# Kernel optimization log

Hardware: AMD Instinct MI355X
Metric: run time of the kernel (lower is better)

The kernel has to match this reference:

```python
import jax, jax.numpy as jnp
import numpy as np

N_NODES = 50000
N_EDGES = 800000
NFEAT, NHID, NCLASS = 256, 64, 2


def _deg_norm(idx, n_nodes, dtype):
    deg = jax.ops.segment_sum(jnp.ones(idx.shape[0], dtype=dtype), idx, num_segments=n_nodes)
    return jax.lax.rsqrt(jnp.maximum(deg, 1.0))


def gcn_layer(x, W, b, src, dst, n_nodes):
    # DGL GraphConv, norm='both': h = D_in^{-1/2} * Agg( D_out^{-1/2} * x ) W + b
    # weight applied before aggregation (in_feats >= out_feats path); math-equivalent.
    norm_src = _deg_norm(src, n_nodes, x.dtype)  # out-degree norm of source nodes
    norm_dst = _deg_norm(dst, n_nodes, x.dtype)  # in-degree norm of dest nodes
    h = (x * norm_src[:, None]) @ W              # [N, out]
    agg = jax.ops.segment_sum(h[src], dst, num_segments=n_nodes)  # gather + scatter-add
    return agg * norm_dst[:, None] + b


def setup_inputs() -> dict:
    key = jax.random.key(0)
    k1, k2, k3, k4, k5, k6, k7 = jax.random.split(key, 7)
    x = jax.random.normal(k1, (N_NODES, NFEAT), dtype=jnp.float32)
    src = jax.random.randint(k2, (N_EDGES,), 0, N_NODES, dtype=jnp.int64)
    dst = jax.random.randint(k3, (N_EDGES,), 0, N_NODES, dtype=jnp.int64)
    # Glorot-style init like DGL GraphConv
    W1 = jax.random.normal(k4, (NFEAT, NHID), dtype=jnp.float32) * (2.0 / (NFEAT + NHID)) ** 0.5
    b1 = jnp.zeros((NHID,), dtype=jnp.float32)
    W2 = jax.random.normal(k5, (NHID, NCLASS), dtype=jnp.float32) * (2.0 / (NHID + NCLASS)) ** 0.5
    b2 = jnp.zeros((NCLASS,), dtype=jnp.float32)
    return {"x": x, "src": src, "dst": dst, "W1": W1, "b1": b1, "W2": W2, "b2": b2}


def reference(x, src, dst, W1, b1, W2, b2):
    h = jax.nn.relu(gcn_layer(x, W1, b1, src, dst, N_NODES))
    # dropout=False -> p=0, no-op
    logits = gcn_layer(h, W2, b2, src, dst, N_NODES)
    return jax.nn.log_softmax(logits, axis=1)
```

## Files before the change

### kernel.cpp

```cpp
#include <hip/hip_runtime.h>
#include <math.h>

#define N_NODES 50000
#define N_EDGES 800000
#define NFEAT 256
#define NHID 64
#define NCLASS 2

#define DB 64
#define NDB 782
#define BCAP 1536
#define EPB 2048
#define NB_EDGE ((N_EDGES + EPB - 1) / EPB)
#define CSTRIDE 32

#define OFF_CURD 0
#define OFF_CURS 25024
#define OFF_RBD  50048
#define OFF_NDST 150048
#define OFF_NSRC 200048
#define OFF_W1T  250048
#define OFF_DPK  258240
#define OFF_SV6  1459392
#define OFF_HB   1759680
#define OFF_H2   3359680

typedef __attribute__((ext_vector_type(8))) short bf16x8;
typedef __attribute__((ext_vector_type(8))) short short8;
typedef __attribute__((ext_vector_type(4))) float f32x4;

static __device__ __forceinline__ unsigned short f2bf(float f) {
    union { float f; unsigned int u; } v; v.f = f;
    return (unsigned short)((v.u + 0x8000u) >> 16);
}
static __device__ __forceinline__ unsigned int pk2bf(float f0, float f1) {
    union { float f; unsigned int u; } a, b; a.f = f0; b.f = f1;
    return __builtin_amdgcn_perm(b.u + 0x8000u, a.u + 0x8000u, 0x07060302u);
}
static __device__ __forceinline__ float bflo(unsigned int u) {
    union { unsigned int x; float f; } v; v.x = u << 16; return v.f;
}
static __device__ __forceinline__ float bfhi(unsigned int u) {
    union { unsigned int x; float f; } v; v.x = u & 0xffff0000u; return v.f;
}

#define INIT_CUR (2 * NDB * CSTRIDE)
#define INIT_N (INIT_CUR + NFEAT * NHID)
__global__ __launch_bounds__(256) void init_kernel(const float* __restrict__ W1,
                                                   int* __restrict__ cursors,
                                                   unsigned short* __restrict__ w1t) {
    int g = blockIdx.x * 256 + threadIdx.x;
    if (g < INIT_CUR) {
        cursors[g] = 0;
    } else if (g < INIT_N) {
        int idx = g - INIT_CUR;
        int k = idx >> 6, n = idx & 63;
        w1t[n * NFEAT + k] = f2bf(W1[idx]);
    }
}

struct SgShared { int hd[NDB], bd[NDB], cd[NDB], hs[NDB], bs[NDB], cs[NDB]; };
__global__ __launch_bounds__(256) void sg_kernel(const int* __restrict__ src,
                                                 const int* __restrict__ dst,
                                                 const float* __restrict__ x,
                                                 const unsigned short* __restrict__ w1t,
                                                 int* __restrict__ cur_d,
                                                 int* __restrict__ cur_s,
                                                 int* __restrict__ dpk,
                                                 unsigned char* __restrict__ sv6,
                                                 unsigned short* __restrict__ hb) {
    __shared__ SgShared su;
    int t = threadIdx.x;
    int bid = blockIdx.x;
    if (bid % 3 == 0) {
        int eb = bid / 3;
        for (int i = t; i < NDB; i += 256) { su.hd[i] = 0; su.cd[i] = 0; su.hs[i] = 0; su.cs[i] = 0; }
        __syncthreads();
        int base = eb * EPB;
        int ls[8], ld[8];
#pragma unroll
        for (int i = 0; i < 8; ++i) {
            int e = base + t + i * 256;
            ls[i] = (e < N_EDGES) ? src[e] : -1;
            ld[i] = (e < N_EDGES) ? dst[e] : -1;
            if (ld[i] >= 0) {
                atomicAdd(&su.hd[ld[i] >> 6], 1);
                atomicAdd(&su.hs[ls[i] >> 6], 1);
            }
        }
        __syncthreads();
        for (int i = t; i < NDB; i += 256) {
            if (su.hd[i]) su.bd[i] = atomicAdd(&cur_d[i * CSTRIDE], su.hd[i]);
            if (su.hs[i]) su.bs[i] = atomicAdd(&cur_s[i * CSTRIDE], su.hs[i]);
        }
        __syncthreads();
#pragma unroll
        for (int i = 0; i < 8; ++i) {
            if (ld[i] >= 0) {
                int bin = ld[i] >> 6;
                int pos = su.bd[bin] + atomicAdd(&su.cd[bin], 1);
                dpk[bin * BCAP + pos] = (ls[i] << 6) | (ld[i] & 63);
                int sbin = ls[i] >> 6;
                int spos = su.bs[sbin] + atomicAdd(&su.cs[sbin], 1);
                sv6[sbin * BCAP + spos] = (unsigned char)(ls[i] & 63);
            }
        }
    } else {
        const int b = (bid / 3) * 2 + (bid % 3) - 1;
        const int row0 = b * 64;
        const int w = t >> 6;
        const int l = t & 63;
        const int m = l & 15;
        const int q = l >> 4;
        int grow = row0 + w * 16 + m;
        const float* xr = &x[(size_t)((grow < N_NODES) ? grow : 0) * NFEAT];
        f32x4 acc[4] = {{0.f, 0.f, 0.f, 0.f}, {0.f, 0.f, 0.f, 0.f},
                        {0.f, 0.f, 0.f, 0.f}, {0.f, 0.f, 0.f, 0.f}};
#pragma unroll
        for (int c8 = 0; c8 < 8; ++c8) {
            int k0 = c8 * 32 + q * 8;
            float4 av0 = *(const float4*)(xr + k0);
            float4 av1 = *(const float4*)(xr + k0 + 4);
            union { bf16x8 v; unsigned int u[4]; } a;
            a.u[0] = pk2bf(av0.x, av0.y);
            a.u[1] = pk2bf(av0.z, av0.w);
            a.u[2] = pk2bf(av1.x, av1.y);
            a.u[3] = pk2bf(av1.z, av1.w);
#pragma unroll
            for (int ct = 0; ct < 4; ++ct) {
                bf16x8 bb = *(const bf16x8*)(&w1t[(ct * 16 + m) * NFEAT + k0]);
                acc[ct] = __builtin_amdgcn_mfma_f32_16x16x32_bf16(a.v, bb, acc[ct], 0, 0, 0);
            }
        }
#pragma unroll
        for (int reg = 0; reg < 4; ++reg) {
            int r = row0 + w * 16 + q * 4 + reg;
            if (r < N_NODES) {
#pragma unroll
                for (int ct = 0; ct < 4; ++ct)
                    hb[(size_t)r * NHID + ct * 16 + m] = f2bf(acc[ct][reg]);
            }
        }
    }
}

union FinShared {
    struct { int ebuf[BCAP]; int hist4[256]; int hist[64]; int seg[64]; int cur[64]; } d;
    struct { int hist4[256]; } s;
};
__global__ __launch_bounds__(256) void fin_kernel(const int* __restrict__ cur_d,
                                                  const int* __restrict__ cur_s,
                                                  const int* __restrict__ dpk,
                                                  const unsigned char* __restrict__ sv6,
                                                  int2* __restrict__ rbdeg,
                                                  float* __restrict__ norm_dst,
                                                  float* __restrict__ norm_src,
                                                  int* __restrict__ csr) {
    __shared__ FinShared su;
    int t = threadIdx.x;
    int role = blockIdx.x & 1;
    int b = blockIdx.x >> 1;

    if (role == 0) {
        su.s.hist4[t] = 0;
        __syncthreads();
        int cnt = cur_s[b * CSTRIDE];
        int base = b * BCAP;
        int sub = (t & 3) * 64;
        for (int j = t; j < cnt; j += 256) atomicAdd(&su.s.hist4[sub + sv6[base + j]], 1);
        __syncthreads();
        if (t < 64) {
            int gid = b * 64 + t;
            if (gid < N_NODES) {
                int v = su.s.hist4[t] + su.s.hist4[64 + t] + su.s.hist4[128 + t] + su.s.hist4[192 + t];
                norm_src[gid] = rsqrtf(fmaxf((float)v, 1.0f));
            }
        }
    } else {
        int cnt = cur_d[b * CSTRIDE];
        int base = b * BCAP;
        if (t < 64) { su.d.hist[t] = 0; su.d.cur[t] = 0; }
        su.d.hist4[t] = 0;
        for (int j = t; j < cnt; j += 256) su.d.ebuf[j] = dpk[base + j];
        __syncthreads();
        int sub = (t & 3) * 64;
        for (int j = t; j < cnt; j += 256) atomicAdd(&su.d.hist4[sub + (su.d.ebuf[j] & 63)], 1);
        __syncthreads();
        if (t < 64) {
            int v = su.d.hist4[t] + su.d.hist4[64 + t] + su.d.hist4[128 + t] + su.d.hist4[192 + t];
            su.d.hist[t] = v;
            su.d.seg[t] = v;
        }
        __syncthreads();
#pragma unroll
        for (int off = 1; off < 64; off <<= 1) {
            int xv = 0;
            if (t < 64 && t >= off) xv = su.d.seg[t - off];
            __syncthreads();
            if (t < 64) su.d.seg[t] += xv;
            __syncthreads();
        }
        if (t < 64) {
            int v = su.d.hist[t];
            int excl = su.d.seg[t] - v;
            int gid = b * 64 + t;
            if (gid < N_NODES) {
                rbdeg[gid] = make_int2(base + excl, v);
                norm_dst[gid] = rsqrtf(fmaxf((float)v, 1.0f));
            }
            su.d.seg[t] = excl;
        }
        __syncthreads();
        for (int j = t; j < cnt; j += 256) {
            int p = su.d.ebuf[j];
            int dlow = p & 63;
            int pos = base + su.d.seg[dlow] + atomicAdd(&su.d.cur[dlow], 1);
            csr[pos] = ((unsigned)p) >> 6;
        }
    }
}

__global__ __launch_bounds__(256) void fused1_kernel(const int2* __restrict__ rbdeg,
                                                     const int* __restrict__ csr,
                                                     const unsigned short* __restrict__ hb,
                                                     const float* __restrict__ norm_dst,
                                                     const float* __restrict__ norm_src,
                                                     const float* __restrict__ b1,
                                                     const float* __restrict__ W2,
                                                     float* __restrict__ h2) {
    int gtid = blockIdx.x * blockDim.x + threadIdx.x;
    int node = gtid >> 6;
    int lane = gtid & 63;
    if (node >= N_NODES) return;
    int e8 = lane >> 3, fg = lane & 7;
    int2 rd = rbdeg[node];
    int beg = rd.x;
    int end = beg + rd.y;
    float a0 = 0.f, a1 = 0.f, a2 = 0.f, a3 = 0.f, a4 = 0.f, a5 = 0.f, a6 = 0.f, a7 = 0.f;
    for (int j = beg; j < end; j += 32) {
        int j0 = j + e8, j1 = j0 + 8, j2 = j0 + 16, j3 = j0 + 24;
        uint4 u0 = make_uint4(0u, 0u, 0u, 0u), u1 = make_uint4(0u, 0u, 0u, 0u);
        uint4 u2 = make_uint4(0u, 0u, 0u, 0u), u3 = make_uint4(0u, 0u, 0u, 0u);
        float ns0 = 0.f, ns1 = 0.f, ns2 = 0.f, ns3 = 0.f;
        if (j0 < end) {
            int s = csr[j0];
            ns0 = norm_src[s];
            u0 = *(const uint4*)(&hb[(size_t)s * NHID + fg * 8]);
        }
        if (j1 < end) {
            int s = csr[j1];
            ns1 = norm_src[s];
            u1 = *(const uint4*)(&hb[(size_t)s * NHID + fg * 8]);
        }
        if (j2 < end) {
            int s = csr[j2];
            ns2 = norm_src[s];
            u2 = *(const uint4*)(&hb[(size_t)s * NHID + fg * 8]);
        }
        if (j3 < end) {
            int s = csr[j3];
            ns3 = norm_src[s];
            u3 = *(const uint4*)(&hb[(size_t)s * NHID + fg * 8]);
        }
        a0 = fmaf(ns0, bflo(u0.x), fmaf(ns1, bflo(u1.x), fmaf(ns2, bflo(u2.x), fmaf(ns3, bflo(u3.x), a0))));
        a1 = fmaf(ns0, bfhi(u0.x), fmaf(ns1, bfhi(u1.x), fmaf(ns2, bfhi(u2.x), fmaf(ns3, bfhi(u3.x), a1))));
        a2 = fmaf(ns0, bflo(u0.y), fmaf(ns1, bflo(u1.y), fmaf(ns2, bflo(u2.y), fmaf(ns3, bflo(u3.y), a2))));
        a3 = fmaf(ns0, bfhi(u0.y), fmaf(ns1, bfhi(u1.y), fmaf(ns2, bfhi(u2.y), fmaf(ns3, bfhi(u3.y), a3))));
        a4 = fmaf(ns0, bflo(u0.z), fmaf(ns1, bflo(u1.z), fmaf(ns2, bflo(u2.z), fmaf(ns3, bflo(u3.z), a4))));
        a5 = fmaf(ns0, bfhi(u0.z), fmaf(ns1, bfhi(u1.z), fmaf(ns2, bfhi(u2.z), fmaf(ns3, bfhi(u3.z), a5))));
        a6 = fmaf(ns0, bflo(u0.w), fmaf(ns1, bflo(u1.w), fmaf(ns2, bflo(u2.w), fmaf(ns3, bflo(u3.w), a6))));
        a7 = fmaf(ns0, bfhi(u0.w), fmaf(ns1, bfhi(u1.w), fmaf(ns2, bfhi(u2.w), fmaf(ns3, bfhi(u3.w), a7))));
    }
#pragma unroll
    for (int off = 8; off <= 32; off <<= 1) {
        a0 += __shfl_xor(a0, off, 64);
        a1 += __shfl_xor(a1, off, 64);
        a2 += __shfl_xor(a2, off, 64);
        a3 += __shfl_xor(a3, off, 64);
        a4 += __shfl_xor(a4, off, 64);
        a5 += __shfl_xor(a5, off, 64);
        a6 += __shfl_xor(a6, off, 64);
        a7 += __shfl_xor(a7, off, 64);
    }
    float nd = norm_dst[node], ns = norm_src[node];
    float4 bv0 = *(const float4*)(&b1[fg * 8]);
    float4 bv1 = *(const float4*)(&b1[fg * 8 + 4]);
    float4 w0 = *(const float4*)(&W2[fg * 16 + 0]);
    float4 w1 = *(const float4*)(&W2[fg * 16 + 4]);
    float4 w2v = *(const float4*)(&W2[fg * 16 + 8]);
    float4 w3 = *(const float4*)(&W2[fg * 16 + 12]);
    float h0 = fmaxf(fmaf(a0, nd, bv0.x), 0.f) * ns;
    float h1 = fmaxf(fmaf(a1, nd, bv0.y), 0.f) * ns;
    float h2f = fmaxf(fmaf(a2, nd, bv0.z), 0.f) * ns;
    float h3 = fmaxf(fmaf(a3, nd, bv0.w), 0.f) * ns;
    float h4 = fmaxf(fmaf(a4, nd, bv1.x), 0.f) * ns;
    float h5 = fmaxf(fmaf(a5, nd, bv1.y), 0.f) * ns;
    float h6 = fmaxf(fmaf(a6, nd, bv1.z), 0.f) * ns;
    float h7 = fmaxf(fmaf(a7, nd, bv1.w), 0.f) * ns;
    float p0 = h0 * w0.x + h1 * w0.z + h2f * w1.x + h3 * w1.z +
               h4 * w2v.x + h5 * w2v.z + h6 * w3.x + h7 * w3.z;
    float p1 = h0 * w0.y + h1 * w0.w + h2f * w1.y + h3 * w1.w +
               h4 * w2v.y + h5 * w2v.w + h6 * w3.y + h7 * w3.w;
#pragma unroll
    for (int off = 1; off <= 4; off <<= 1) {
        p0 += __shfl_xor(p0, off, 64);
        p1 += __shfl_xor(p1, off, 64);
    }
    if (lane == 0) *(float2*)(&h2[node * 2]) = make_float2(p0, p1);
}

__global__ __launch_bounds__(256) void fused2_kernel(const int2* __restrict__ rbdeg,
                                                     const int* __restrict__ csr,
                                                     const float* __restrict__ h2,
                                                     const float* __restrict__ norm_dst,
                                                     const float* __restrict__ b2,
                                                     float* __restrict__ out) {
    int gtid = blockIdx.x * blockDim.x + threadIdx.x;
    int n = gtid >> 4;
    int l16 = gtid & 15;
    if (n >= N_NODES) return;
    int2 rd = rbdeg[n];
    int beg = rd.x, end = rd.x + rd.y;
    float s0 = 0.f, s1 = 0.f;
    for (int j = beg + l16; j < end; j += 16) {
        float2 v = *(const float2*)(&h2[csr[j] * 2]);
        s0 += v.x;
        s1 += v.y;
    }
#pragma unroll
    for (int off = 1; off <= 8; off <<= 1) {
        s0 += __shfl_xor(s0, off, 16);
        s1 += __shfl_xor(s1, off, 16);
    }
    if (l16 == 0) {
        float nd = norm_dst[n];
        float l0 = fmaf(s0, nd, b2[0]);
        float l1 = fmaf(s1, nd, b2[1]);
        float m = fmaxf(l0, l1);
        float lse = m + logf(expf(l0 - m) + expf(l1 - m));
        *(float2*)(&out[n * 2]) = make_float2(l0 - lse, l1 - lse);
    }
}

extern "C" void kernel_launch(void* const* d_in, const int* in_sizes, int n_in,
                              void* d_out, int out_size, void* d_ws, size_t ws_size,
                              hipStream_t stream) {
    const float* x  = (const float*)d_in[0];
    const int* src  = (const int*)d_in[1];
    const int* dst  = (const int*)d_in[2];
    const float* W1 = (const float*)d_in[3];
    const float* b1 = (const float*)d_in[4];
    const float* W2 = (const float*)d_in[5];
    const float* b2 = (const float*)d_in[6];
    float* out = (float*)d_out;
    float* ws  = (float*)d_ws;
    int*   wsi = (int*)d_ws;

    int*   cur_d    = wsi + OFF_CURD;
    int*   cur_s    = wsi + OFF_CURS;
    int2*  rbdeg    = (int2*)(wsi + OFF_RBD);
    float* norm_dst = ws + OFF_NDST;
    float* norm_src = ws + OFF_NSRC;
    unsigned short* w1t = (unsigned short*)(wsi + OFF_W1T);
    int*   dpk      = wsi + OFF_DPK;
    unsigned char* sv6 = (unsigned char*)(wsi + OFF_SV6);
    int*   csr      = wsi + OFF_DPK;
    unsigned short* hb = (unsigned short*)(wsi + OFF_HB);
    float* h2       = ws + OFF_H2;

    init_kernel<<<(INIT_N + 255) / 256, 256, 0, stream>>>(W1, cur_d, w1t);
    sg_kernel<<<NB_EDGE * 3, 256, 0, stream>>>(src, dst, x, w1t, cur_d, cur_s, dpk, sv6, hb);
    fin_kernel<<<NDB * 2, 256, 0, stream>>>(cur_d, cur_s, dpk, sv6, rbdeg, norm_dst, norm_src, csr);
    {
        long long threads = (long long)N_NODES * 64;
        fused1_kernel<<<(int)((threads + 255) / 256), 256, 0, stream>>>(
            rbdeg, csr, hb, norm_dst, norm_src, b1, W2, h2);
    }
    {
        long long threads = (long long)N_NODES * 16;
        fused2_kernel<<<(int)((threads + 255) / 256), 256, 0, stream>>>(
            rbdeg, csr, h2, norm_dst, b2, out);
    }
}
```

Baseline: 178.4 us.

## Split GEMM out of scatter kernel and fold source norm into GEMM output

The combined scatter+GEMM kernel is split back into a pure edge-scatter kernel and a separate GEMM kernel that runs after degree finalization. That lets the GEMM multiply each row by norm_src before storing hb, so the aggregation loop drops the per-edge norm_src gather and FMAs in favour of plain adds. The GEMM also preloads all x row data into registers and uses smaller 128-thread blocks, and the scatter's global cursor atomics are issued in a batched, unrolled form. The cost is one extra kernel launch and losing the overlap of GEMM with the edge scatter.

```diff
diff --git a/kernel.cpp b/kernel.cpp
--- a/kernel.cpp
+++ b/kernel.cpp
@@ -26,7 +26,6 @@
 #define OFF_H2   3359680
 
 typedef __attribute__((ext_vector_type(8))) short bf16x8;
-typedef __attribute__((ext_vector_type(8))) short short8;
 typedef __attribute__((ext_vector_type(4))) float f32x4;
 
 static __device__ __forceinline__ unsigned short f2bf(float f) {
@@ -60,86 +59,60 @@
 }
 
 struct SgShared { int hd[NDB], bd[NDB], cd[NDB], hs[NDB], bs[NDB], cs[NDB]; };
-__global__ __launch_bounds__(256) void sg_kernel(const int* __restrict__ src,
-                                                 const int* __restrict__ dst,
-                                                 const float* __restrict__ x,
-                                                 const unsigned short* __restrict__ w1t,
-                                                 int* __restrict__ cur_d,
-                                                 int* __restrict__ cur_s,
-                                                 int* __restrict__ dpk,
-                                                 unsigned char* __restrict__ sv6,
-                                                 unsigned short* __restrict__ hb) {
+__global__ __launch_bounds__(256) void scatter_kernel(const int* __restrict__ src,
+                                                      const int* __restrict__ dst,
+                                                      int* __restrict__ cur_d,
+                                                      int* __restrict__ cur_s,
+                                                      int* __restrict__ dpk,
+                                                      unsigned char* __restrict__ sv6) {
     __shared__ SgShared su;
     int t = threadIdx.x;
-    int bid = blockIdx.x;
-    if (bid % 3 == 0) {
-        int eb = bid / 3;
-        for (int i = t; i < NDB; i += 256) { su.hd[i] = 0; su.cd[i] = 0; su.hs[i] = 0; su.cs[i] = 0; }
-        __syncthreads();
-        int base = eb * EPB;
-        int ls[8], ld[8];
-#pragma unroll
-        for (int i = 0; i < 8; ++i) {
-            int e = base + t + i * 256;
-            ls[i] = (e < N_EDGES) ? src[e] : -1;
-            ld[i] = (e < N_EDGES) ? dst[e] : -1;
-            if (ld[i] >= 0) {
-                atomicAdd(&su.hd[ld[i] >> 6], 1);
-                atomicAdd(&su.hs[ls[i] >> 6], 1);
-            }
-        }
-        __syncthreads();
-        for (int i = t; i < NDB; i += 256) {
-            if (su.hd[i]) su.bd[i] = atomicAdd(&cur_d[i * CSTRIDE], su.hd[i]);
-            if (su.hs[i]) su.bs[i] = atomicAdd(&cur_s[i * CSTRIDE], su.hs[i]);
-        }
-        __syncthreads();
-#pragma unroll
-        for (int i = 0; i < 8; ++i) {
-            if (ld[i] >= 0) {
-                int bin = ld[i] >> 6;
-                int pos = su.bd[bin] + atomicAdd(&su.cd[bin], 1);
-                dpk[bin * BCAP + pos] = (ls[i] << 6) | (ld[i] & 63);
-                int sbin = ls[i] >> 6;
-                int spos = su.bs[sbin] + atomicAdd(&su.cs[sbin], 1);
-                sv6[sbin * BCAP + spos] = (unsigned char)(ls[i] & 63);
-            }
-        }
-    } else {
-        const int b = (bid / 3) * 2 + (bid % 3) - 1;
-        const int row0 = b * 64;
-        const int w = t >> 6;
-        const int l = t & 63;
-        const int m = l & 15;
-        const int q = l >> 4;
-        int grow = row0 + w * 16 + m;
-        const float* xr = &x[(size_t)((grow < N_NODES) ? grow : 0) * NFEAT];
-        f32x4 acc[4] = {{0.f, 0.f, 0.f, 0.f}, {0.f, 0.f, 0.f, 0.f},
-                        {0.f, 0.f, 0.f, 0.f}, {0.f, 0.f, 0.f, 0.f}};
-#pragma unroll
-        for (int c8 = 0; c8 < 8; ++c8) {
-            int k0 = c8 * 32 + q * 8;
-            float4 av0 = *(const float4*)(xr + k0);
-            float4 av1 = *(const float4*)(xr + k0 + 4);
-            union { bf16x8 v; unsigned int u[4]; } a;
-            a.u[0] = pk2bf(av0.x, av0.y);
-            a.u[1] = pk2bf(av0.z, av0.w);
-            a.u[2] = pk2bf(av1.x, av1.y);
-            a.u[3] = pk2bf(av1.z, av1.w);
-#pragma unroll
-            for (int ct = 0; ct < 4; ++ct) {
-                bf16x8 bb = *(const bf16x8*)(&w1t[(ct * 16 + m) * NFEAT + k0]);
-                acc[ct] = __builtin_amdgcn_mfma_f32_16x16x32_bf16(a.v, bb, acc[ct], 0, 0, 0);
-            }
-        }
-#pragma unroll
-        for (int reg = 0; reg < 4; ++reg) {
-            int r = row0 + w * 16 + q * 4 + reg;
-            if (r < N_NODES) {
-#pragma unroll
-                for (int ct = 0; ct < 4; ++ct)
-                    hb[(size_t)r * NHID + ct * 16 + m] = f2bf(acc[ct][reg]);
-            }
+    for (int i = t; i < NDB; i += 256) { su.hd[i] = 0; su.cd[i] = 0; su.hs[i] = 0; su.cs[i] = 0; }
+    __syncthreads();
+    int base = blockIdx.x * EPB;
+    int ls[8], ld[8];
+#pragma unroll
+    for (int i = 0; i < 8; ++i) {
+        int e = base + t + i * 256;
+        ls[i] = (e < N_EDGES) ? src[e] : -1;
+        ld[i] = (e < N_EDGES) ? dst[e] : -1;
+        if (ld[i] >= 0) {
+            atomicAdd(&su.hd[ld[i] >> 6], 1);
+            atomicAdd(&su.hs[ls[i] >> 6], 1);
+        }
+    }
+    __syncthreads();
+    {
+        int i0 = t, i1 = t + 256, i2 = t + 512, i3 = t + 768;
+        int hd0 = su.hd[i0], hs0 = su.hs[i0];
+        int hd1 = su.hd[i1], hs1 = su.hs[i1];
+        int hd2 = su.hd[i2], hs2 = su.hs[i2];
+        int hd3 = (i3 < NDB) ? su.hd[i3] : 0;
+        int hs3 = (i3 < NDB) ? su.hs[i3] : 0;
+        int b0 = 0, b1v = 0, b2v = 0, b3v = 0, c0 = 0, c1v = 0, c2v = 0, c3v = 0;
+        if (hd0) b0  = atomicAdd(&cur_d[i0 * CSTRIDE], hd0);
+        if (hs0) c0  = atomicAdd(&cur_s[i0 * CSTRIDE], hs0);
+        if (hd1) b1v = atomicAdd(&cur_d[i1 * CSTRIDE], hd1);
+        if (hs1) c1v = atomicAdd(&cur_s[i1 * CSTRIDE], hs1);
+        if (hd2) b2v = atomicAdd(&cur_d[i2 * CSTRIDE], hd2);
+        if (hs2) c2v = atomicAdd(&cur_s[i2 * CSTRIDE], hs2);
+        if (hd3) b3v = atomicAdd(&cur_d[i3 * CSTRIDE], hd3);
+        if (hs3) c3v = atomicAdd(&cur_s[i3 * CSTRIDE], hs3);
+        su.bd[i0] = b0;  su.bs[i0] = c0;
+        su.bd[i1] = b1v; su.bs[i1] = c1v;
+        su.bd[i2] = b2v; su.bs[i2] = c2v;
+        if (i3 < NDB) { su.bd[i3] = b3v; su.bs[i3] = c3v; }
+    }
+    __syncthreads();
+#pragma unroll
+    for (int i = 0; i < 8; ++i) {
+        if (ld[i] >= 0) {
+            int bin = ld[i] >> 6;
+            int pos = su.bd[bin] + atomicAdd(&su.cd[bin], 1);
+            dpk[bin * BCAP + pos] = (ls[i] << 6) | (ld[i] & 63);
+            int sbin = ls[i] >> 6;
+            int spos = su.bs[sbin] + atomicAdd(&su.cs[sbin], 1);
+            sv6[sbin * BCAP + spos] = (unsigned char)(ls[i] & 63);
         }
     }
 }
@@ -217,6 +190,50 @@
             int pos = base + su.d.seg[dlow] + atomicAdd(&su.d.cur[dlow], 1);
             csr[pos] = ((unsigned)p) >> 6;
         }
+    }
+}
+
+__global__ __launch_bounds__(128, 3) void gemm_kernel(const float* __restrict__ x,
+                                                      const unsigned short* __restrict__ w1t,
+                                                      const float* __restrict__ norm_src,
+                                                      unsigned short* __restrict__ hb) {
+    int t = threadIdx.x;
+    int w = t >> 6;
+    int l = t & 63;
+    int m = l & 15;
+    int q = l >> 4;
+    int base = (blockIdx.x * 2 + w) * 16;
+    if (base >= N_NODES) return;
+    const float* xr = &x[(size_t)(base + m) * NFEAT];
+    float4 av[16];
+#pragma unroll
+    for (int i = 0; i < 8; ++i) {
+        av[2 * i]     = *(const float4*)(xr + i * 32 + q * 8);
+        av[2 * i + 1] = *(const float4*)(xr + i * 32 + q * 8 + 4);
+    }
+    f32x4 acc[4] = {{0.f, 0.f, 0.f, 0.f}, {0.f, 0.f, 0.f, 0.f},
+                    {0.f, 0.f, 0.f, 0.f}, {0.f, 0.f, 0.f, 0.f}};
+#pragma unroll
+    for (int c8 = 0; c8 < 8; ++c8) {
+        int k0 = c8 * 32 + q * 8;
+        union { bf16x8 v; unsigned int u[4]; } a;
+        a.u[0] = pk2bf(av[2 * c8].x, av[2 * c8].y);
+        a.u[1] = pk2bf(av[2 * c8].z, av[2 * c8].w);
+        a.u[2] = pk2bf(av[2 * c8 + 1].x, av[2 * c8 + 1].y);
+        a.u[3] = pk2bf(av[2 * c8 + 1].z, av[2 * c8 + 1].w);
+#pragma unroll
+        for (int ct = 0; ct < 4; ++ct) {
+            bf16x8 bb = *(const bf16x8*)(&w1t[(ct * 16 + m) * NFEAT + k0]);
+            acc[ct] = __builtin_amdgcn_mfma_f32_16x16x32_bf16(a.v, bb, acc[ct], 0, 0, 0);
+        }
+    }
+#pragma unroll
+    for (int reg = 0; reg < 4; ++reg) {
+        int r = base + q * 4 + reg;
+        float ns = norm_src[r];
+#pragma unroll
+        for (int ct = 0; ct < 4; ++ct)
+            hb[(size_t)r * NHID + ct * 16 + m] = f2bf(acc[ct][reg] * ns);
     }
 }
 
@@ -241,35 +258,18 @@
         int j0 = j + e8, j1 = j0 + 8, j2 = j0 + 16, j3 = j0 + 24;
         uint4 u0 = make_uint4(0u, 0u, 0u, 0u), u1 = make_uint4(0u, 0u, 0u, 0u);
         uint4 u2 = make_uint4(0u, 0u, 0u, 0u), u3 = make_uint4(0u, 0u, 0u, 0u);
-        float ns0 = 0.f, ns1 = 0.f, ns2 = 0.f, ns3 = 0.f;
-        if (j0 < end) {
-            int s = csr[j0];
-            ns0 = norm_src[s];
-            u0 = *(const uint4*)(&hb[(size_t)s * NHID + fg * 8]);
-        }
-        if (j1 < end) {
-            int s = csr[j1];
-            ns1 = norm_src[s];
-            u1 = *(const uint4*)(&hb[(size_t)s * NHID + fg * 8]);
-        }
-        if (j2 < end) {
-            int s = csr[j2];
-            ns2 = norm_src[s];
-            u2 = *(const uint4*)(&hb[(size_t)s * NHID + fg * 8]);
-        }
-        if (j3 < end) {
-            int s = csr[j3];
-            ns3 = norm_src[s];
-            u3 = *(const uint4*)(&hb[(size_t)s * NHID + fg * 8]);
-        }
-        a0 = fmaf(ns0, bflo(u0.x), fmaf(ns1, bflo(u1.x), fmaf(ns2, bflo(u2.x), fmaf(ns3, bflo(u3.x), a0))));
-        a1 = fmaf(ns0, bfhi(u0.x), fmaf(ns1, bfhi(u1.x), fmaf(ns2, bfhi(u2.x), fmaf(ns3, bfhi(u3.x), a1))));
-        a2 = fmaf(ns0, bflo(u0.y), fmaf(ns1, bflo(u1.y), fmaf(ns2, bflo(u2.y), fmaf(ns3, bflo(u3.y), a2))));
-        a3 = fmaf(ns0, bfhi(u0.y), fmaf(ns1, bfhi(u1.y), fmaf(ns2, bfhi(u2.y), fmaf(ns3, bfhi(u3.y), a3))));
-        a4 = fmaf(ns0, bflo(u0.z), fmaf(ns1, bflo(u1.z), fmaf(ns2, bflo(u2.z), fmaf(ns3, bflo(u3.z), a4))));
-        a5 = fmaf(ns0, bfhi(u0.z), fmaf(ns1, bfhi(u1.z), fmaf(ns2, bfhi(u2.z), fmaf(ns3, bfhi(u3.z), a5))));
-        a6 = fmaf(ns0, bflo(u0.w), fmaf(ns1, bflo(u1.w), fmaf(ns2, bflo(u2.w), fmaf(ns3, bflo(u3.w), a6))));
-        a7 = fmaf(ns0, bfhi(u0.w), fmaf(ns1, bfhi(u1.w), fmaf(ns2, bfhi(u2.w), fmaf(ns3, bfhi(u3.w), a7))));
+        if (j0 < end) u0 = *(const uint4*)(&hb[(size_t)csr[j0] * NHID + fg * 8]);
+        if (j1 < end) u1 = *(const uint4*)(&hb[(size_t)csr[j1] * NHID + fg * 8]);
+        if (j2 < end) u2 = *(const uint4*)(&hb[(size_t)csr[j2] * NHID + fg * 8]);
+        if (j3 < end) u3 = *(const uint4*)(&hb[(size_t)csr[j3] * NHID + fg * 8]);
+        a0 += bflo(u0.x) + bflo(u1.x) + bflo(u2.x) + bflo(u3.x);
+        a1 += bfhi(u0.x) + bfhi(u1.x) + bfhi(u2.x) + bfhi(u3.x);
+        a2 += bflo(u0.y) + bflo(u1.y) + bflo(u2.y) + bflo(u3.y);
+        a3 += bfhi(u0.y) + bfhi(u1.y) + bfhi(u2.y) + bfhi(u3.y);
+        a4 += bflo(u0.z) + bflo(u1.z) + bflo(u2.z) + bflo(u3.z);
+        a5 += bfhi(u0.z) + bfhi(u1.z) + bfhi(u2.z) + bfhi(u3.z);
+        a6 += bflo(u0.w) + bflo(u1.w) + bflo(u2.w) + bflo(u3.w);
+        a7 += bfhi(u0.w) + bfhi(u1.w) + bfhi(u2.w) + bfhi(u3.w);
     }
 #pragma unroll
     for (int off = 8; off <= 32; off <<= 1) {
@@ -369,8 +369,12 @@
     float* h2       = ws + OFF_H2;
 
     init_kernel<<<(INIT_N + 255) / 256, 256, 0, stream>>>(W1, cur_d, w1t);
-    sg_kernel<<<NB_EDGE * 3, 256, 0, stream>>>(src, dst, x, w1t, cur_d, cur_s, dpk, sv6, hb);
+    scatter_kernel<<<NB_EDGE, 256, 0, stream>>>(src, dst, cur_d, cur_s, dpk, sv6);
     fin_kernel<<<NDB * 2, 256, 0, stream>>>(cur_d, cur_s, dpk, sv6, rbdeg, norm_dst, norm_src, csr);
+    {
+        int tiles = (N_NODES + 15) / 16;
+        gemm_kernel<<<(tiles + 1) / 2, 128, 0, stream>>>(x, w1t, norm_src, hb);
+    }
     {
         long long threads = (long long)N_NODES * 64;
         fused1_kernel<<<(int)((threads + 255) / 256), 256, 0, stream>>>(
```

After: 196.8 us. 1.1x slower.

## Shard global bin cursors into 16 sub-buckets to cut atomic contention

Applied to the files above, without the earlier changes.

Each edge-chunk block now reserves space in one of 16 per-bin sub-buckets, picked by chunk index, so contended global atomics on the 782 bin cursors are spread over 16 times more addresses. The finalize kernel gathers the sub-buckets back into a contiguous shared buffer before building the CSR. The CSR gets its own workspace region instead of aliasing dpk, which enlarges the workspace. The GEMM branch also issues all x-row loads up front to raise memory-level parallelism. Sub-bucket counts are clamped to a fixed capacity, so unusually skewed bins could silently drop edges.

```diff
diff --git a/kernel.cpp b/kernel.cpp
--- a/kernel.cpp
+++ b/kernel.cpp
@@ -12,21 +12,24 @@
 #define BCAP 1536
 #define EPB 2048
 #define NB_EDGE ((N_EDGES + EPB - 1) / EPB)
-#define CSTRIDE 32
+#define NSUB 16
+#define SUBCAP 160
+#define SUBREG (NSUB * SUBCAP)
+#define CSTR 8
 
 #define OFF_CURD 0
-#define OFF_CURS 25024
-#define OFF_RBD  50048
-#define OFF_NDST 150048
-#define OFF_NSRC 200048
-#define OFF_W1T  250048
-#define OFF_DPK  258240
-#define OFF_SV6  1459392
-#define OFF_HB   1759680
-#define OFF_H2   3359680
+#define OFF_CURS 100096
+#define OFF_RBD  200192
+#define OFF_NDST 300192
+#define OFF_NSRC 350192
+#define OFF_W1T  400192
+#define OFF_DPK  408384
+#define OFF_SV6  2410304
+#define OFF_CSR  2910784
+#define OFF_HB   4111936
+#define OFF_H2   5711936
 
 typedef __attribute__((ext_vector_type(8))) short bf16x8;
-typedef __attribute__((ext_vector_type(8))) short short8;
 typedef __attribute__((ext_vector_type(4))) float f32x4;
 
 static __device__ __forceinline__ unsigned short f2bf(float f) {
@@ -44,7 +47,7 @@
     union { unsigned int x; float f; } v; v.x = u & 0xffff0000u; return v.f;
 }
 
-#define INIT_CUR (2 * NDB * CSTRIDE)
+#define INIT_CUR (2 * NDB * NSUB * CSTR)
 #define INIT_N (INIT_CUR + NFEAT * NHID)
 __global__ __launch_bounds__(256) void init_kernel(const float* __restrict__ W1,
                                                    int* __restrict__ cursors,
@@ -73,10 +76,11 @@
     int t = threadIdx.x;
     int bid = blockIdx.x;
     if (bid % 3 == 0) {
-        int eb = bid / 3;
+        int chunk = bid / 3;
+        int sub = chunk & (NSUB - 1);
         for (int i = t; i < NDB; i += 256) { su.hd[i] = 0; su.cd[i] = 0; su.hs[i] = 0; su.cs[i] = 0; }
         __syncthreads();
-        int base = eb * EPB;
+        int base = chunk * EPB;
         int ls[8], ld[8];
 #pragma unroll
         for (int i = 0; i < 8; ++i) {
@@ -90,8 +94,8 @@
         }
         __syncthreads();
         for (int i = t; i < NDB; i += 256) {
-            if (su.hd[i]) su.bd[i] = atomicAdd(&cur_d[i * CSTRIDE], su.hd[i]);
-            if (su.hs[i]) su.bs[i] = atomicAdd(&cur_s[i * CSTRIDE], su.hs[i]);
+            if (su.hd[i]) su.bd[i] = atomicAdd(&cur_d[(sub * NDB + i) * CSTR], su.hd[i]);
+            if (su.hs[i]) su.bs[i] = atomicAdd(&cur_s[(sub * NDB + i) * CSTR], su.hs[i]);
         }
         __syncthreads();
 #pragma unroll
@@ -99,10 +103,10 @@
             if (ld[i] >= 0) {
                 int bin = ld[i] >> 6;
                 int pos = su.bd[bin] + atomicAdd(&su.cd[bin], 1);
-                dpk[bin * BCAP + pos] = (ls[i] << 6) | (ld[i] & 63);
+                dpk[(bin * NSUB + sub) * SUBCAP + pos] = (ls[i] << 6) | (ld[i] & 63);
                 int sbin = ls[i] >> 6;
                 int spos = su.bs[sbin] + atomicAdd(&su.cs[sbin], 1);
-                sv6[sbin * BCAP + spos] = (unsigned char)(ls[i] & 63);
+                sv6[(sbin * NSUB + sub) * SUBCAP + spos] = (unsigned char)(ls[i] & 63);
             }
         }
     } else {
@@ -114,18 +118,22 @@
         const int q = l >> 4;
         int grow = row0 + w * 16 + m;
         const float* xr = &x[(size_t)((grow < N_NODES) ? grow : 0) * NFEAT];
+        float4 av[16];
+#pragma unroll
+        for (int i = 0; i < 8; ++i) {
+            av[2 * i]     = *(const float4*)(xr + i * 32 + q * 8);
+            av[2 * i + 1] = *(const float4*)(xr + i * 32 + q * 8 + 4);
+        }
         f32x4 acc[4] = {{0.f, 0.f, 0.f, 0.f}, {0.f, 0.f, 0.f, 0.f},
                         {0.f, 0.f, 0.f, 0.f}, {0.f, 0.f, 0.f, 0.f}};
 #pragma unroll
         for (int c8 = 0; c8 < 8; ++c8) {
             int k0 = c8 * 32 + q * 8;
-            float4 av0 = *(const float4*)(xr + k0);
-            float4 av1 = *(const float4*)(xr + k0 + 4);
             union { bf16x8 v; unsigned int u[4]; } a;
-            a.u[0] = pk2bf(av0.x, av0.y);
-            a.u[1] = pk2bf(av0.z, av0.w);
-            a.u[2] = pk2bf(av1.x, av1.y);
-            a.u[3] = pk2bf(av1.z, av1.w);
+            a.u[0] = pk2bf(av[2 * c8].x, av[2 * c8].y);
+            a.u[1] = pk2bf(av[2 * c8].z, av[2 * c8].w);
+            a.u[2] = pk2bf(av[2 * c8 + 1].x, av[2 * c8 + 1].y);
+            a.u[3] = pk2bf(av[2 * c8 + 1].z, av[2 * c8 + 1].w);
 #pragma unroll
             for (int ct = 0; ct < 4; ++ct) {
                 bf16x8 bb = *(const bf16x8*)(&w1t[(ct * 16 + m) * NFEAT + k0]);
@@ -164,10 +172,13 @@
     if (role == 0) {
         su.s.hist4[t] = 0;
         __syncthreads();
-        int cnt = cur_s[b * CSTRIDE];
-        int base = b * BCAP;
-        int sub = (t & 3) * 64;
-        for (int j = t; j < cnt; j += 256) atomicAdd(&su.s.hist4[sub + sv6[base + j]], 1);
+        int sub4 = (t & 3) * 64;
+        for (int sub = 0; sub < NSUB; ++sub) {
+            int c = cur_s[(sub * NDB + b) * CSTR];
+            c = (c < SUBCAP) ? c : SUBCAP;
+            int gb = (b * NSUB + sub) * SUBCAP;
+            for (int j = t; j < c; j += 256) atomicAdd(&su.s.hist4[sub4 + sv6[gb + j]], 1);
+        }
         __syncthreads();
         if (t < 64) {
             int gid = b * 64 + t;
@@ -177,14 +188,21 @@
             }
         }
     } else {
-        int cnt = cur_d[b * CSTRIDE];
         int base = b * BCAP;
         if (t < 64) { su.d.hist[t] = 0; su.d.cur[t] = 0; }
         su.d.hist4[t] = 0;
-        for (int j = t; j < cnt; j += 256) su.d.ebuf[j] = dpk[base + j];
-        __syncthreads();
-        int sub = (t & 3) * 64;
-        for (int j = t; j < cnt; j += 256) atomicAdd(&su.d.hist4[sub + (su.d.ebuf[j] & 63)], 1);
+        int off = 0;
+        for (int sub = 0; sub < NSUB; ++sub) {
+            int c = cur_d[(sub * NDB + b) * CSTR];
+            c = (c < SUBCAP) ? c : SUBCAP;
+            int gb = (b * NSUB + sub) * SUBCAP;
+            for (int j = t; j < c; j += 256) su.d.ebuf[off + j] = dpk[gb + j];
+            off += c;
+        }
+        int cnt = off;
+        __syncthreads();
+        int sub4 = (t & 3) * 64;
+        for (int j = t; j < cnt; j += 256) atomicAdd(&su.d.hist4[sub4 + (su.d.ebuf[j] & 63)], 1);
         __syncthreads();
         if (t < 64) {
             int v = su.d.hist4[t] + su.d.hist4[64 + t] + su.d.hist4[128 + t] + su.d.hist4[192 + t];
@@ -193,9 +211,9 @@
         }
         __syncthreads();
 #pragma unroll
-        for (int off = 1; off < 64; off <<= 1) {
+        for (int offp = 1; offp < 64; offp <<= 1) {
             int xv = 0;
-            if (t < 64 && t >= off) xv = su.d.seg[t - off];
+            if (t < 64 && t >= offp) xv = su.d.seg[t - offp];
             __syncthreads();
             if (t < 64) su.d.seg[t] += xv;
             __syncthreads();
@@ -364,7 +382,7 @@
     unsigned short* w1t = (unsigned short*)(wsi + OFF_W1T);
     int*   dpk      = wsi + OFF_DPK;
     unsigned char* sv6 = (unsigned char*)(wsi + OFF_SV6);
-    int*   csr      = wsi + OFF_DPK;
+    int*   csr      = wsi + OFF_CSR;
     unsigned short* hb = (unsigned short*)(wsi + OFF_HB);
     float* h2       = ws + OFF_H2;
 
```

Measured after the change: 170.6 us. 1.05x faster.
